# Kernel optimization log

Measured on AMD Instinct MI355X. Metric: run time of the kernel, lower is better.

## Reference

```python
import jax, jax.numpy as jnp
import numpy as np

IMG = 224
PATCH_SIZE = 2      # stride of the output patch grid (output_size = H // PATCH_SIZE)
PATCH_PIXEL = 4     # samples per patch side (deformable resampling resolution)
EMBED = 192
OFFSET_EMBED = 2    # (dx, dy) per patch
IN_CH = 3
BATCH = 32


def setup_inputs() -> dict:
    key = jax.random.key(0)
    k1, k2, k3 = jax.random.split(key, 3)
    x = jax.random.normal(k1, (BATCH, IN_CH, IMG, IMG), jnp.float32)
    conv_w = jax.random.normal(k2, (EMBED, IN_CH, 3, 3), jnp.float32) * 0.05
    conv_b = jnp.zeros((EMBED,), jnp.float32)
    off_w = jax.random.normal(k3, (OFFSET_EMBED, EMBED), jnp.float32) * 0.02
    return {"x": x, "conv_w": conv_w, "conv_b": conv_b, "off_w": off_w}


def _bilinear_gather(img, ys, xs):
    # img: [B, C, H, W]; ys, xs: [B, P] float pixel coords. Border-clamped bilinear.
    B, C, H, W = img.shape
    y0 = jnp.floor(ys)
    x0 = jnp.floor(xs)
    wy = (ys - y0)[:, None, :]
    wx = (xs - x0)[:, None, :]
    y0i = jnp.clip(y0.astype(jnp.int32), 0, H - 1)
    y1i = jnp.clip(y0i + 1, 0, H - 1)
    x0i = jnp.clip(x0.astype(jnp.int32), 0, W - 1)
    x1i = jnp.clip(x0i + 1, 0, W - 1)
    flat = img.reshape(B, C, H * W)
    P = ys.shape[1]

    def g(yi, xi):
        idx = (yi * W + xi)[:, None, :]  # [B,1,P]
        return jnp.take_along_axis(flat, jnp.broadcast_to(idx, (B, C, P)), axis=2)

    v00 = g(y0i, x0i)
    v01 = g(y0i, x1i)
    v10 = g(y1i, x0i)
    v11 = g(y1i, x1i)
    return (v00 * (1 - wy) * (1 - wx) + v01 * (1 - wy) * wx
            + v10 * wy * (1 - wx) + v11 * wy * wx)  # [B,C,P]


def reference(x, conv_w, conv_b, off_w):
    B, C, H, W = x.shape
    # PatchEmbed: conv k3 s2 p1 -> flatten -> tokens [B, N, E]
    feat = jax.lax.conv_general_dilated(
        x, conv_w, window_strides=(2, 2), padding=((1, 1), (1, 1)),
        dimension_numbers=('NCHW', 'OIHW', 'NCHW')) + conv_b[None, :, None, None]
    Hf, Wf = feat.shape[2], feat.shape[3]
    tokens = feat.reshape(B, EMBED, Hf * Wf).transpose(0, 2, 1)  # [B,N,E]
    # offset predictor: GELU (exact) then bias-free linear
    pred = jax.nn.gelu(tokens, approximate=False) @ off_w.T      # [B,N,2]

    Ho, Wo = H // PATCH_SIZE, W // PATCH_SIZE  # == (Hf, Wf) by construction
    off = pred.reshape(B, Ho, Wo, OFFSET_EMBED) * PATCH_SIZE     # pixel-space offsets

    # Deformable patch resampling: each output patch samples a PATCH_PIXEL^2 grid
    # centered at its shifted patch center.
    cy = (jnp.arange(Ho, dtype=jnp.float32) + 0.5) * PATCH_SIZE
    cx = (jnp.arange(Wo, dtype=jnp.float32) + 0.5) * PATCH_SIZE
    local = ((jnp.arange(PATCH_PIXEL, dtype=jnp.float32) + 0.5) / PATCH_PIXEL
             * PATCH_SIZE - PATCH_SIZE / 2)
    ys = (cy[None, :, None, None, None] + off[..., 1][:, :, :, None, None]
          + local[None, None, None, :, None])
    xs = (cx[None, None, :, None, None] + off[..., 0][:, :, :, None, None]
          + local[None, None, None, None, :])
    shape5 = (B, Ho, Wo, PATCH_PIXEL, PATCH_PIXEL)
    ys = jnp.broadcast_to(ys, shape5).reshape(B, -1)
    xs = jnp.broadcast_to(xs, shape5).reshape(B, -1)

    sampled = _bilinear_gather(x, ys, xs)  # [B,C,Ho*Wo*pp*pp]
    out = sampled.reshape(B, C, Ho, Wo, PATCH_PIXEL, PATCH_PIXEL)
    out = out.transpose(0, 1, 2, 4, 3, 5).reshape(
        B, C, Ho * PATCH_PIXEL, Wo * PATCH_PIXEL)
    return out
```

## Files before the change

### kernel.cpp

```cpp
#include <hip/hip_runtime.h>

#define IMG   224
#define IMG2  (IMG * IMG)
#define HO    112
#define WO_   112
#define EMBED 192
#define BATCH 32
#define PPB   (HO * WO_)
#define NPOS  (BATCH * PPB)

typedef __attribute__((ext_vector_type(8))) short short8;
typedef __attribute__((ext_vector_type(4))) float float4v;
typedef __attribute__((ext_vector_type(2))) float float2v;

__device__ __forceinline__ short f2bf(float f) {
    unsigned u = __builtin_bit_cast(unsigned, f);
    u += 0x7FFFu + ((u >> 16) & 1u);
    return (short)(u >> 16);
}

__device__ __forceinline__ float fast_gelu(float a) {
    float e = __builtin_amdgcn_exp2f(a * -2.45546507f);
    return a * __builtin_amdgcn_rcpf(1.0f + e);
}

__device__ __forceinline__ void tile_offsets(
    const float* __restrict__ xb,
    const short8* __restrict__ bfrag,
    const float* __restrict__ owx, const float* __restrict__ owy,
    const int* __restrict__ offj, const bool* __restrict__ isr,
    const bool* __restrict__ k27,
    int ho, int wo0, int col, int quad,
    float ox[4], float oy[4])
{
    int iy0 = 2 * ho - 1;
    int ixl = 2 * (wo0 + col) - 1;
    int base = iy0 * IMG + ixl;

    short8 a;
    if (ho > 0 && wo0 > 0) {
#pragma unroll
        for (int j = 0; j < 8; ++j) {
            float v = isr[j] ? xb[base + offj[j]] : 0.0f;
            if (k27[j]) v = 1.0f;
            a[j] = f2bf(v);
        }
    } else {
#pragma unroll
        for (int j = 0; j < 8; ++j) {
            int k  = quad * 8 + j;
            int r9 = k % 9;
            int dy = r9 / 3, dx = r9 % 3;
            bool ok = isr[j] && (iy0 + dy >= 0) && (ixl + dx >= 0);
            int ad = ok ? (base + offj[j]) : 0;
            float v = ok ? xb[ad] : 0.0f;
            if (k27[j]) v = 1.0f;
            a[j] = f2bf(v);
        }
    }

    ox[0] = ox[1] = ox[2] = ox[3] = 0.0f;
    oy[0] = oy[1] = oy[2] = oy[3] = 0.0f;
#pragma unroll
    for (int nt = 0; nt < 12; ++nt) {
        float4v c = {0.0f, 0.0f, 0.0f, 0.0f};
        c = __builtin_amdgcn_mfma_f32_16x16x32_bf16(a, bfrag[nt], c, 0, 0, 0);
#pragma unroll
        for (int r = 0; r < 4; ++r) {
            float g = fast_gelu(c[r]);
            ox[r] = fmaf(g, owx[nt], ox[r]);
            oy[r] = fmaf(g, owy[nt], oy[r]);
        }
    }
#pragma unroll
    for (int d = 1; d < 16; d <<= 1) {
#pragma unroll
        for (int r = 0; r < 4; ++r) {
            ox[r] += __shfl_xor(ox[r], d, 64);
            oy[r] += __shfl_xor(oy[r], d, 64);
        }
    }
}

__device__ __forceinline__ void resample_patch(
    const float* __restrict__ xb, float* __restrict__ ob,
    int ho, int wo, int px, float ofx, float ofy)
{
    float xs  = 2.0f * wo + 0.25f + 0.5f * px + ofx;
    float x0f = floorf(xs);
    float wx  = xs - x0f;
    int x0 = (int)x0f; x0 = min(max(x0, 0), IMG - 1);
    int xq = min(x0, IMG - 2);
    bool selx = (x0 > xq);
    int ocol = wo * 4 + px;

#pragma unroll
    for (int py = 0; py < 4; ++py) {
        float ys  = 2.0f * ho + 0.25f + 0.5f * py + ofy;
        float y0f = floorf(ys);
        float wy  = ys - y0f;
        int y0 = (int)y0f; y0 = min(max(y0, 0), IMG - 1);
        int dyo = (y0 < IMG - 1) ? IMG : 0;
        int rb = y0 * IMG + xq;
        int orow = (ho * 4 + py) * 448 + ocol;

#pragma unroll
        for (int c = 0; c < 3; ++c) {
            int v0 = rb + c * IMG2;
            int v1 = v0 + dyo;
            float A0 = xb[v0], A1 = xb[v0 + 1];
            float B0 = xb[v1], B1 = xb[v1 + 1];
            float v00 = selx ? A1 : A0;
            float v10 = selx ? B1 : B0;
            float top = fmaf(wx, A1 - v00, v00);
            float bot = fmaf(wx, B1 - v10, v10);
            ob[c * 200704 + orow] = fmaf(wy, bot - top, top);
        }
    }
}

__global__ __launch_bounds__(128)
void offsets_kernel(const float* __restrict__ x,
                    const float* __restrict__ conv_w,
                    const float* __restrict__ conv_b,
                    const float* __restrict__ off_w,
                    float2v* __restrict__ offs) {
    const int lane = threadIdx.x & 63;
    const int wv   = threadIdx.x >> 6;
    const int col  = lane & 15;
    const int quad = lane >> 4;

    const int b   = blockIdx.x / (PPB / 128);
    const int pb0 = (blockIdx.x % (PPB / 128)) * 128 + wv * 64;
    const float* __restrict__ xb = x + (size_t)b * 3 * IMG2;

    int  offj[8];
    bool isr[8], k27[8];
#pragma unroll
    for (int j = 0; j < 8; ++j) {
        int k = quad * 8 + j;
        int c = k / 9, r9 = k % 9;
        int dy = r9 / 3, dx = r9 % 3;
        isr[j] = (k < 27);
        k27[j] = (k == 27);
        offj[j] = isr[j] ? (c * IMG2 + dy * IMG + dx) : 0;
    }

    short8 bfrag[12];
#pragma unroll
    for (int nt = 0; nt < 12; ++nt) {
        int ch = nt * 16 + col;
#pragma unroll
        for (int j = 0; j < 8; ++j) {
            int k = quad * 8 + j;
            float v = (k < 27) ? conv_w[ch * 27 + k]
                               : ((k == 27) ? conv_b[ch] : 0.0f);
            bfrag[nt][j] = f2bf(v);
        }
    }
    float owx[12], owy[12];
#pragma unroll
    for (int nt = 0; nt < 12; ++nt) {
        owx[nt] = off_w[nt * 16 + col] * 2.0f;
        owy[nt] = off_w[EMBED + nt * 16 + col] * 2.0f;
    }

    for (int it = 0; it < 4; ++it) {
        int p   = pb0 + it * 16;
        int ho  = p / WO_;
        int wo0 = p % WO_;

        float ox[4], oy[4];
        tile_offsets(xb, bfrag, owx, owy, offj, isr, k27,
                     ho, wo0, col, quad, ox, oy);

        int rsel = col & 3;
        float sx01 = (rsel & 1) ? ox[1] : ox[0];
        float sx23 = (rsel & 1) ? ox[3] : ox[2];
        float vx   = (rsel & 2) ? sx23 : sx01;
        float sy01 = (rsel & 1) ? oy[1] : oy[0];
        float sy23 = (rsel & 1) ? oy[3] : oy[2];
        float vy   = (rsel & 2) ? sy23 : sy01;
        if (col < 4) {
            int gpos = blockIdx.x * 128 + wv * 64 + it * 16 + quad * 4 + rsel;
            float2v o; o[0] = vx; o[1] = vy;
            offs[gpos] = o;
        }
    }
}

__global__ __launch_bounds__(256, 8)
void resample_kernel(const float* __restrict__ x,
                     const float2v* __restrict__ offs,
                     float* __restrict__ out) {
    const int lane  = threadIdx.x & 63;
    const int wv    = threadIdx.x >> 6;
    const int patch = lane >> 2;
    const int px    = lane & 3;

    const int b  = blockIdx.x / (PPB / 64);
    const int sb = (blockIdx.x % (PPB / 64)) * 64 + wv * 16;
    const int ho  = sb / WO_;
    const int wo0 = sb % WO_;

    const float* __restrict__ xb = x + (size_t)b * 3 * IMG2;
    float* __restrict__ ob = out + (size_t)b * 3 * (448 * 448);

    float2v o = offs[blockIdx.x * 64 + wv * 16 + patch];
    resample_patch(xb, ob, ho, wo0 + patch, px, o[0], o[1]);
}

__global__ __launch_bounds__(128)
void fused_kernel(const float* __restrict__ x,
                  const float* __restrict__ conv_w,
                  const float* __restrict__ conv_b,
                  const float* __restrict__ off_w,
                  float* __restrict__ out) {
    const int lane = threadIdx.x & 63;
    const int wv   = threadIdx.x >> 6;
    const int col  = lane & 15;
    const int quad = lane >> 4;

    const int b   = blockIdx.x / (PPB / 128);
    const int pb0 = (blockIdx.x % (PPB / 128)) * 128 + wv * 64;
    const float* __restrict__ xb = x + (size_t)b * 3 * IMG2;
    float* __restrict__ ob = out + (size_t)b * 3 * (448 * 448);

    int  offj[8];
    bool isr[8], k27[8];
#pragma unroll
    for (int j = 0; j < 8; ++j) {
        int k = quad * 8 + j;
        int c = k / 9, r9 = k % 9;
        int dy = r9 / 3, dx = r9 % 3;
        isr[j] = (k < 27);
        k27[j] = (k == 27);
        offj[j] = isr[j] ? (c * IMG2 + dy * IMG + dx) : 0;
    }
    short8 bfrag[12];
#pragma unroll
    for (int nt = 0; nt < 12; ++nt) {
        int ch = nt * 16 + col;
#pragma unroll
        for (int j = 0; j < 8; ++j) {
            int k = quad * 8 + j;
            float v = (k < 27) ? conv_w[ch * 27 + k]
                               : ((k == 27) ? conv_b[ch] : 0.0f);
            bfrag[nt][j] = f2bf(v);
        }
    }
    float owx[12], owy[12];
#pragma unroll
    for (int nt = 0; nt < 12; ++nt) {
        owx[nt] = off_w[nt * 16 + col] * 2.0f;
        owy[nt] = off_w[EMBED + nt * 16 + col] * 2.0f;
    }

    for (int it = 0; it < 4; ++it) {
        int p   = pb0 + it * 16;
        int ho  = p / WO_;
        int wo0 = p % WO_;

        float ox[4], oy[4];
        tile_offsets(xb, bfrag, owx, owy, offj, isr, k27,
                     ho, wo0, col, quad, ox, oy);

        int patch = lane >> 2;
        int rsel  = patch & 3;
        int px    = lane & 3;
        float sx01 = (rsel & 1) ? ox[1] : ox[0];
        float sx23 = (rsel & 1) ? ox[3] : ox[2];
        float ofx  = (rsel & 2) ? sx23 : sx01;
        float sy01 = (rsel & 1) ? oy[1] : oy[0];
        float sy23 = (rsel & 1) ? oy[3] : oy[2];
        float ofy  = (rsel & 2) ? sy23 : sy01;

        resample_patch(xb, ob, ho, wo0 + patch, px, ofx, ofy);
    }
}

extern "C" void kernel_launch(void* const* d_in, const int* in_sizes, int n_in,
                              void* d_out, int out_size, void* d_ws, size_t ws_size,
                              hipStream_t stream) {
    const float* x      = (const float*)d_in[0];
    const float* conv_w = (const float*)d_in[1];
    const float* conv_b = (const float*)d_in[2];
    const float* off_w  = (const float*)d_in[3];
    float* out = (float*)d_out;

    const size_t need = (size_t)NPOS * sizeof(float2v);
    if (d_ws != nullptr && ws_size >= need) {
        float2v* offs = (float2v*)d_ws;
        offsets_kernel<<<NPOS / 128, 128, 0, stream>>>(x, conv_w, conv_b, off_w, offs);
        resample_kernel<<<NPOS / 64, 256, 0, stream>>>(x, offs, out);
    } else {
        fused_kernel<<<NPOS / 128, 128, 0, stream>>>(x, conv_w, conv_b, off_w, out);
    }
}
```

Before: 154.8 us.

## Compute offset projection with a second MFMA and transpose conv tile

The offsets kernel now computes the conv as the transposed product (channels by positions), applies GELU, and packs the result directly into bf16 B-fragments for a second MFMA that carries the 192-to-2 offset projection. This replaces the per-lane FMA accumulation and the 16-lane shuffle reduction. It also switches to packed bf16 conversion instructions and uses 256 threads per block with half as many tiles per wave. The cost is that GELU outputs and offset weights are rounded to bf16, which can perturb the offsets slightly.

```diff
diff --git a/kernel.cpp b/kernel.cpp
--- a/kernel.cpp
+++ b/kernel.cpp
@@ -12,6 +12,7 @@
 typedef __attribute__((ext_vector_type(8))) short short8;
 typedef __attribute__((ext_vector_type(4))) float float4v;
 typedef __attribute__((ext_vector_type(2))) float float2v;
+typedef __attribute__((ext_vector_type(4))) unsigned uint4v;
 
 __device__ __forceinline__ short f2bf(float f) {
     unsigned u = __builtin_bit_cast(unsigned, f);
@@ -19,67 +20,15 @@
     return (short)(u >> 16);
 }
 
+__device__ __forceinline__ unsigned cvt_pk_bf16(float lo, float hi) {
+    unsigned r;
+    asm("v_cvt_pk_bf16_f32 %0, %1, %2" : "=v"(r) : "v"(lo), "v"(hi));
+    return r;
+}
+
 __device__ __forceinline__ float fast_gelu(float a) {
     float e = __builtin_amdgcn_exp2f(a * -2.45546507f);
     return a * __builtin_amdgcn_rcpf(1.0f + e);
-}
-
-__device__ __forceinline__ void tile_offsets(
-    const float* __restrict__ xb,
-    const short8* __restrict__ bfrag,
-    const float* __restrict__ owx, const float* __restrict__ owy,
-    const int* __restrict__ offj, const bool* __restrict__ isr,
-    const bool* __restrict__ k27,
-    int ho, int wo0, int col, int quad,
-    float ox[4], float oy[4])
-{
-    int iy0 = 2 * ho - 1;
-    int ixl = 2 * (wo0 + col) - 1;
-    int base = iy0 * IMG + ixl;
-
-    short8 a;
-    if (ho > 0 && wo0 > 0) {
-#pragma unroll
-        for (int j = 0; j < 8; ++j) {
-            float v = isr[j] ? xb[base + offj[j]] : 0.0f;
-            if (k27[j]) v = 1.0f;
-            a[j] = f2bf(v);
-        }
-    } else {
-#pragma unroll
-        for (int j = 0; j < 8; ++j) {
-            int k  = quad * 8 + j;
-            int r9 = k % 9;
-            int dy = r9 / 3, dx = r9 % 3;
-            bool ok = isr[j] && (iy0 + dy >= 0) && (ixl + dx >= 0);
-            int ad = ok ? (base + offj[j]) : 0;
-            float v = ok ? xb[ad] : 0.0f;
-            if (k27[j]) v = 1.0f;
-            a[j] = f2bf(v);
-        }
-    }
-
-    ox[0] = ox[1] = ox[2] = ox[3] = 0.0f;
-    oy[0] = oy[1] = oy[2] = oy[3] = 0.0f;
-#pragma unroll
-    for (int nt = 0; nt < 12; ++nt) {
-        float4v c = {0.0f, 0.0f, 0.0f, 0.0f};
-        c = __builtin_amdgcn_mfma_f32_16x16x32_bf16(a, bfrag[nt], c, 0, 0, 0);
-#pragma unroll
-        for (int r = 0; r < 4; ++r) {
-            float g = fast_gelu(c[r]);
-            ox[r] = fmaf(g, owx[nt], ox[r]);
-            oy[r] = fmaf(g, owy[nt], oy[r]);
-        }
-    }
-#pragma unroll
-    for (int d = 1; d < 16; d <<= 1) {
-#pragma unroll
-        for (int r = 0; r < 4; ++r) {
-            ox[r] += __shfl_xor(ox[r], d, 64);
-            oy[r] += __shfl_xor(oy[r], d, 64);
-        }
-    }
 }
 
 __device__ __forceinline__ void resample_patch(
@@ -119,7 +68,7 @@
     }
 }
 
-__global__ __launch_bounds__(128)
+__global__ __launch_bounds__(256, 4)
 void offsets_kernel(const float* __restrict__ x,
                     const float* __restrict__ conv_w,
                     const float* __restrict__ conv_b,
@@ -131,7 +80,7 @@
     const int quad = lane >> 4;
 
     const int b   = blockIdx.x / (PPB / 128);
-    const int pb0 = (blockIdx.x % (PPB / 128)) * 128 + wv * 64;
+    const int pb0 = (blockIdx.x % (PPB / 128)) * 128 + wv * 32;
     const float* __restrict__ xb = x + (size_t)b * 3 * IMG2;
 
     int  offj[8];
@@ -158,32 +107,72 @@
             bfrag[nt][j] = f2bf(v);
         }
     }
-    float owx[12], owy[12];
-#pragma unroll
-    for (int nt = 0; nt < 12; ++nt) {
-        owx[nt] = off_w[nt * 16 + col] * 2.0f;
-        owy[nt] = off_w[EMBED + nt * 16 + col] * 2.0f;
-    }
-
-    for (int it = 0; it < 4; ++it) {
+
+    short8 a2[6];
+#pragma unroll
+    for (int nt2 = 0; nt2 < 6; ++nt2) {
+#pragma unroll
+        for (int j = 0; j < 8; ++j) {
+            int ch = nt2 * 32 + ((j < 4) ? (quad * 4 + j)
+                                         : (16 + quad * 4 + (j - 4)));
+            float w = (col < 2) ? off_w[col * EMBED + ch] * 2.0f : 0.0f;
+            a2[nt2][j] = f2bf(w);
+        }
+    }
+
+#pragma unroll
+    for (int it = 0; it < 2; ++it) {
         int p   = pb0 + it * 16;
         int ho  = p / WO_;
         int wo0 = p % WO_;
-
-        float ox[4], oy[4];
-        tile_offsets(xb, bfrag, owx, owy, offj, isr, k27,
-                     ho, wo0, col, quad, ox, oy);
-
-        int rsel = col & 3;
-        float sx01 = (rsel & 1) ? ox[1] : ox[0];
-        float sx23 = (rsel & 1) ? ox[3] : ox[2];
-        float vx   = (rsel & 2) ? sx23 : sx01;
-        float sy01 = (rsel & 1) ? oy[1] : oy[0];
-        float sy23 = (rsel & 1) ? oy[3] : oy[2];
-        float vy   = (rsel & 2) ? sy23 : sy01;
-        if (col < 4) {
-            int gpos = blockIdx.x * 128 + wv * 64 + it * 16 + quad * 4 + rsel;
-            float2v o; o[0] = vx; o[1] = vy;
+        int iy0 = 2 * ho - 1;
+        int ixl = 2 * (wo0 + col) - 1;
+        int base = iy0 * IMG + ixl;
+
+        float v[8];
+        if (ho > 0 && wo0 > 0) {
+#pragma unroll
+            for (int j = 0; j < 8; ++j) {
+                float t = isr[j] ? xb[base + offj[j]] : 0.0f;
+                v[j] = k27[j] ? 1.0f : t;
+            }
+        } else {
+#pragma unroll
+            for (int j = 0; j < 8; ++j) {
+                int k  = quad * 8 + j;
+                int r9 = k % 9;
+                int dy = r9 / 3, dx = r9 % 3;
+                bool ok = isr[j] && (iy0 + dy >= 0) && (ixl + dx >= 0);
+                int ad = ok ? (base + offj[j]) : 0;
+                float t = ok ? xb[ad] : 0.0f;
+                v[j] = k27[j] ? 1.0f : t;
+            }
+        }
+        uint4v au = {cvt_pk_bf16(v[0], v[1]), cvt_pk_bf16(v[2], v[3]),
+                     cvt_pk_bf16(v[4], v[5]), cvt_pk_bf16(v[6], v[7])};
+        short8 afrag = __builtin_bit_cast(short8, au);
+
+        float4v c2 = {0.0f, 0.0f, 0.0f, 0.0f};
+#pragma unroll
+        for (int nt2 = 0; nt2 < 6; ++nt2) {
+            float4v z = {0.0f, 0.0f, 0.0f, 0.0f};
+            float4v ca = __builtin_amdgcn_mfma_f32_16x16x32_bf16(
+                             bfrag[2 * nt2],     afrag, z, 0, 0, 0);
+            float4v cb = __builtin_amdgcn_mfma_f32_16x16x32_bf16(
+                             bfrag[2 * nt2 + 1], afrag, z, 0, 0, 0);
+            uint4v gt = {cvt_pk_bf16(fast_gelu(ca[0]), fast_gelu(ca[1])),
+                         cvt_pk_bf16(fast_gelu(ca[2]), fast_gelu(ca[3])),
+                         cvt_pk_bf16(fast_gelu(cb[0]), fast_gelu(cb[1])),
+                         cvt_pk_bf16(fast_gelu(cb[2]), fast_gelu(cb[3]))};
+            short8 gb = __builtin_bit_cast(short8, gt);
+            c2 = __builtin_amdgcn_mfma_f32_16x16x32_bf16(a2[nt2], gb, c2, 0, 0, 0);
+        }
+
+        if (quad == 0) {
+            int gpos = blockIdx.x * 128 + wv * 32 + it * 16 + col;
+            float2v o;
+            o[0] = c2[0];
+            o[1] = c2[1];
             offs[gpos] = o;
         }
     }
@@ -260,10 +249,52 @@
         int p   = pb0 + it * 16;
         int ho  = p / WO_;
         int wo0 = p % WO_;
-
-        float ox[4], oy[4];
-        tile_offsets(xb, bfrag, owx, owy, offj, isr, k27,
-                     ho, wo0, col, quad, ox, oy);
+        int iy0 = 2 * ho - 1;
+        int ixl = 2 * (wo0 + col) - 1;
+        int base = iy0 * IMG + ixl;
+
+        short8 a;
+        if (ho > 0 && wo0 > 0) {
+#pragma unroll
+            for (int j = 0; j < 8; ++j) {
+                float v = isr[j] ? xb[base + offj[j]] : 0.0f;
+                if (k27[j]) v = 1.0f;
+                a[j] = f2bf(v);
+            }
+        } else {
+#pragma unroll
+            for (int j = 0; j < 8; ++j) {
+                int k  = quad * 8 + j;
+                int r9 = k % 9;
+                int dy = r9 / 3, dx = r9 % 3;
+                bool ok = isr[j] && (iy0 + dy >= 0) && (ixl + dx >= 0);
+                int ad = ok ? (base + offj[j]) : 0;
+                float v = ok ? xb[ad] : 0.0f;
+                if (k27[j]) v = 1.0f;
+                a[j] = f2bf(v);
+            }
+        }
+
+        float ox[4] = {0, 0, 0, 0}, oy[4] = {0, 0, 0, 0};
+#pragma unroll
+        for (int nt = 0; nt < 12; ++nt) {
+            float4v c = {0.0f, 0.0f, 0.0f, 0.0f};
+            c = __builtin_amdgcn_mfma_f32_16x16x32_bf16(a, bfrag[nt], c, 0, 0, 0);
+#pragma unroll
+            for (int r = 0; r < 4; ++r) {
+                float g = fast_gelu(c[r]);
+                ox[r] = fmaf(g, owx[nt], ox[r]);
+                oy[r] = fmaf(g, owy[nt], oy[r]);
+            }
+        }
+#pragma unroll
+        for (int d = 1; d < 16; d <<= 1) {
+#pragma unroll
+            for (int r = 0; r < 4; ++r) {
+                ox[r] += __shfl_xor(ox[r], d, 64);
+                oy[r] += __shfl_xor(oy[r], d, 64);
+            }
+        }
 
         int patch = lane >> 2;
         int rsel  = patch & 3;
@@ -291,7 +322,7 @@
     const size_t need = (size_t)NPOS * sizeof(float2v);
     if (d_ws != nullptr && ws_size >= need) {
         float2v* offs = (float2v*)d_ws;
-        offsets_kernel<<<NPOS / 128, 128, 0, stream>>>(x, conv_w, conv_b, off_w, offs);
+        offsets_kernel<<<NPOS / 128, 256, 0, stream>>>(x, conv_w, conv_b, off_w, offs);
         resample_kernel<<<NPOS / 64, 256, 0, stream>>>(x, offs, out);
     } else {
         fused_kernel<<<NPOS / 128, 128, 0, stream>>>(x, conv_w, conv_b, off_w, out);
```

Result: slower. 272.7 us (+76.2%).
